# Kernel optimization log

Measured on AMD Instinct MI355X. Metric: run time of the kernel, lower is better.

## Reference

```python
import jax, jax.numpy as jnp
import numpy as np

N = 100000   # nodes
E = 3200000  # edges
D = 128      # in_channels
H = 128      # subhiddens
O = 128      # out_channels
S = 2048     # subgraphs
EPS = 1e-5


def _glorot(k, shape):
    lim = np.sqrt(6.0 / (shape[0] + shape[1])).astype(np.float32)
    return jax.random.uniform(k, shape, jnp.float32, -lim, lim)


def setup_inputs() -> dict:
    key = jax.random.key(0)
    ks = jax.random.split(key, 8)
    x = jax.random.normal(ks[0], (N, D), jnp.float32)
    edge_index = jax.random.randint(ks[1], (2, E), 0, N, dtype=jnp.int32)
    node_to_subgraph = jnp.sort(jax.random.randint(ks[2], (N,), 0, S, dtype=jnp.int32))
    return {
        "x": x,
        "edge_index": edge_index,
        "node_to_subgraph": node_to_subgraph,
        "W1": _glorot(ks[3], (D, H)), "b1": jnp.zeros((H,), jnp.float32),
        "g1": jnp.ones((H,), jnp.float32), "be1": jnp.zeros((H,), jnp.float32),
        "W2": _glorot(ks[4], (H, H)), "b2": jnp.zeros((H,), jnp.float32),
        "g2": jnp.ones((H,), jnp.float32), "be2": jnp.zeros((H,), jnp.float32),
        "W3": _glorot(ks[5], (H, O)), "b3": jnp.zeros((O,), jnp.float32),
    }


def _gcn_conv(x, W, b, row, col, norm):
    # PyG GCNConv: out[col] += norm * (x @ W)[row], then + bias.
    xw = x @ W                                    # [N+?, d] -> [N, d_out]
    msg = xw[row] * norm[:, None]                 # gather over source nodes
    out = jax.ops.segment_sum(msg, col, num_segments=N)
    return out + b


def _bn_relu(x, g, be):
    # BatchNorm1d (training-mode batch stats, biased var) + ReLU
    mean = jnp.mean(x, axis=0)
    var = jnp.mean(jnp.square(x - mean), axis=0)
    return jax.nn.relu((x - mean) * jax.lax.rsqrt(var + EPS) * g + be)


def reference(x, edge_index, node_to_subgraph, W1, b1, g1, be1, W2, b2, g2, be2, W3, b3):
    # GCN symmetric norm with self-loops, shared across the 3 convs.
    loops = jnp.arange(N, dtype=edge_index.dtype)
    row = jnp.concatenate([edge_index[0], loops])  # source
    col = jnp.concatenate([edge_index[1], loops])  # target (aggregation)
    deg = jax.ops.segment_sum(jnp.ones_like(col, dtype=x.dtype), col, num_segments=N)
    dinv = jnp.where(deg > 0, jax.lax.rsqrt(deg), 0.0)
    norm = dinv[row] * dinv[col]

    h1 = _bn_relu(_gcn_conv(x, W1, b1, row, col, norm), g1, be1)   # dropout is no-op in eval
    h2 = _bn_relu(_gcn_conv(h1, W2, b2, row, col, norm), g2, be2)
    h3 = jax.nn.relu(_gcn_conv(h2, W3, b3, row, col, norm))

    cat = jnp.concatenate([h1, h2, h3], axis=-1)                   # [N, 2H+O]
    return jax.ops.segment_max(cat, node_to_subgraph, num_segments=S)  # gmp -> [S, 2H+O]
```

## Files before the change

### kernel.cpp

```cpp
#include <hip/hip_runtime.h>
#include <hip/hip_fp16.h>

#define NN 100000
#define NE 3200000
#define DF 128
#define SG 2048
#define OUTC 384
#define EPS 1e-5f

#define NBUK 800
#define BNODES 125
#define CAP 5120
#define TILE 4096
#define B_BUCKET 782
#define B_GEMM 391
#define LDSTRIDE 136
#define AGG_BLOCKS 2048

typedef _Float16 f16x8 __attribute__((ext_vector_type(8)));
typedef float f32x16 __attribute__((ext_vector_type(16)));

__global__ void k_prepW(const float* __restrict__ W1, const float* __restrict__ W2,
                        const float* __restrict__ W3, __half* __restrict__ WT) {
    const float* W = blockIdx.x == 0 ? W1 : (blockIdx.x == 1 ? W2 : W3);
    __half* out = WT + blockIdx.x * 16384;
    for (int i = threadIdx.x; i < 16384; i += 256) {
        int k = i >> 7, n = i & 127;
        out[n * 128 + k] = __float2half(W[i]);
    }
}

__device__ void bucketA_body(int* smem, int bb,
                             const int* __restrict__ erow, const int* __restrict__ ecol,
                             int* __restrict__ gcur, int* __restrict__ packed) {
    int* sc   = smem;
    int* sr   = smem + 4096;
    int* hist = smem + 8192;
    int* loff = smem + 9216;
    int* gch  = smem + 10240;
    int* cur  = smem + 11264;
    int* psum = smem + 12288;
    int t = threadIdx.x;
    hist[t] = 0; hist[t + 256] = 0; hist[t + 512] = 0; hist[t + 768] = 0;
    __syncthreads();
    int e0 = bb * TILE;
    int lim = NE - e0; if (lim > TILE) lim = TILE;
    for (int i = t; i < lim; i += 256) {
        int c = ecol[e0 + i];
        int r = erow[e0 + i];
        sc[i] = c; sr[i] = r;
        atomicAdd(&hist[c / BNODES], 1);
    }
    __syncthreads();
    int h0 = hist[4 * t], h1 = hist[4 * t + 1], h2 = hist[4 * t + 2], h3 = hist[4 * t + 3];
    int s = h0 + h1 + h2 + h3;
    psum[t] = s; __syncthreads();
    for (int st = 1; st < 256; st <<= 1) {
        int a = (t >= st) ? psum[t - st] : 0;
        __syncthreads();
        psum[t] += a;
        __syncthreads();
    }
    int base = psum[t] - s;
    loff[4 * t] = base;
    loff[4 * t + 1] = base + h0;
    loff[4 * t + 2] = base + h0 + h1;
    loff[4 * t + 3] = base + h0 + h1 + h2;
#pragma unroll
    for (int j = 0; j < 4; ++j) {
        int b = 4 * t + j;
        if (b < NBUK) {
            int c = hist[b];
            gch[b] = c ? atomicAdd(&gcur[b], c) : 0;
            cur[b] = loff[b];
        }
    }
    __syncthreads();
    for (int i = t; i < lim; i += 256) {
        int c = sc[i], r = sr[i];
        int b = c / BNODES;
        int lc = c - b * BNODES;
        int p = atomicAdd(&cur[b], 1);
        int rank = p - loff[b];
        if (gch[b] + rank < CAP) packed[b * CAP + gch[b] + rank] = r | (lc << 17);
    }
}

__device__ void gemm32u_body(int* smem, int gb, const float* __restrict__ A,
                             const __half* __restrict__ WTg, __half* __restrict__ C) {
    _Float16* Wl = (_Float16*)smem;
    int tid = threadIdx.x;
    for (int ch = tid; ch < 2048; ch += 256) {
        int n = ch >> 4, seg = ch & 15;
        *(uint4*)&Wl[n * LDSTRIDE + seg * 8] = *(const uint4*)(WTg + n * 128 + seg * 8);
    }
    __syncthreads();
    int wave = tid >> 6, lane = tid & 63;
    int l31 = lane & 31, lhi = lane >> 5;
    int rowbase = gb * 256 + wave * 64;
    f32x16 acc[2][4];
#pragma unroll
    for (int rt = 0; rt < 2; ++rt)
#pragma unroll
        for (int nt = 0; nt < 4; ++nt)
#pragma unroll
            for (int i = 0; i < 16; ++i) acc[rt][nt][i] = 0.f;
    int r0 = rowbase + l31;      if (r0 >= NN) r0 = NN - 1;
    int r1 = rowbase + 32 + l31; if (r1 >= NN) r1 = NN - 1;
    const float* A0 = A + (size_t)r0 * 128;
    const float* A1 = A + (size_t)r1 * 128;
#pragma unroll
    for (int ks = 0; ks < 8; ++ks) {
        int koff = ks * 16 + lhi * 8;
        float4 f0 = *(const float4*)(A0 + koff);
        float4 f1 = *(const float4*)(A0 + koff + 4);
        float4 g0 = *(const float4*)(A1 + koff);
        float4 g1 = *(const float4*)(A1 + koff + 4);
        f16x8 a0, a1;
        a0[0] = (_Float16)f0.x; a0[1] = (_Float16)f0.y; a0[2] = (_Float16)f0.z; a0[3] = (_Float16)f0.w;
        a0[4] = (_Float16)f1.x; a0[5] = (_Float16)f1.y; a0[6] = (_Float16)f1.z; a0[7] = (_Float16)f1.w;
        a1[0] = (_Float16)g0.x; a1[1] = (_Float16)g0.y; a1[2] = (_Float16)g0.z; a1[3] = (_Float16)g0.w;
        a1[4] = (_Float16)g1.x; a1[5] = (_Float16)g1.y; a1[6] = (_Float16)g1.z; a1[7] = (_Float16)g1.w;
#pragma unroll
        for (int nt = 0; nt < 4; ++nt) {
            f16x8 b = *(const f16x8*)&Wl[(nt * 32 + l31) * LDSTRIDE + ks * 16 + lhi * 8];
            acc[0][nt] = __builtin_amdgcn_mfma_f32_32x32x16_f16(a0, b, acc[0][nt], 0, 0, 0);
            acc[1][nt] = __builtin_amdgcn_mfma_f32_32x32x16_f16(a1, b, acc[1][nt], 0, 0, 0);
        }
    }
#pragma unroll
    for (int rt = 0; rt < 2; ++rt) {
#pragma unroll
        for (int r = 0; r < 16; ++r) {
            int row = rowbase + rt * 32 + (r & 3) + 8 * (r >> 2) + 4 * lhi;
            if (row < NN) {
                size_t cb = (size_t)row * 128 + l31;
                C[cb]      = __float2half(acc[rt][0][r]);
                C[cb + 32] = __float2half(acc[rt][1][r]);
                C[cb + 64] = __float2half(acc[rt][2][r]);
                C[cb + 96] = __float2half(acc[rt][3][r]);
            }
        }
    }
}

__global__ __launch_bounds__(256, 2) void k_fused1(const int* __restrict__ erow,
                                                   const int* __restrict__ ecol,
                                                   int* __restrict__ gcur,
                                                   int* __restrict__ packed,
                                                   const float* __restrict__ x,
                                                   const __half* __restrict__ WT,
                                                   __half* __restrict__ XWh) {
    __shared__ __align__(16) int smem[12544];
    int bb = blockIdx.x;
    if (bb < B_BUCKET) bucketA_body(smem, bb, erow, ecol, gcur, packed);
    else gemm32u_body(smem, bb - B_BUCKET, x, WT, XWh);
}

__global__ __launch_bounds__(256) void k_csrB(int* __restrict__ rows,
                                              const int* __restrict__ gcur,
                                              int* __restrict__ begs, int* __restrict__ ends,
                                              float* __restrict__ dinv) {
    __shared__ int lin[CAP];
    __shared__ int hist[128], off[128], cur[128], psc[128];
    int b = blockIdx.x, t = threadIdx.x;
    int cnt = gcur[b]; if (cnt > CAP) cnt = CAP;
    int base = b * CAP;
    for (int i = t; i < cnt; i += 256) lin[i] = rows[base + i];
    if (t < 128) hist[t] = 0;
    __syncthreads();
    for (int i = t; i < cnt; i += 256) atomicAdd(&hist[lin[i] >> 17], 1);
    __syncthreads();
    int pc = 0;
    if (t < 128) { pc = (hist[t] + 3) & ~3; psc[t] = pc; }
    __syncthreads();
    for (int st = 1; st < 128; st <<= 1) {
        int a = 0;
        if (t < 128 && t >= st) a = psc[t - st];
        __syncthreads();
        if (t < 128) psc[t] += a;
        __syncthreads();
    }
    if (t < 128) { off[t] = psc[t] - pc; cur[t] = off[t]; }
    __syncthreads();
    if (t < BNODES) {
        int n = b * BNODES + t;
        int c = hist[t];
        int bg = base + off[t];
        begs[n] = bg;
        ends[n] = bg + c;
        dinv[n] = rsqrtf((float)(c + 1));
        int pad = (c + 3) & ~3;
        for (int p = c; p < pad; ++p)
            if (off[t] + p < CAP) rows[base + off[t] + p] = 0;
    }
    __syncthreads();
    for (int i = t; i < cnt; i += 256) {
        int w = lin[i];
        int lc = w >> 17;
        int p = atomicAdd(&cur[lc], 1);
        if (p < CAP) rows[base + p] = w & 0x1FFFF;
    }
}

__global__ __launch_bounds__(256, 2) void k_gemm16(const __half* __restrict__ A,
                                                   const __half* __restrict__ WTg,
                                                   const float* __restrict__ dinv,
                                                   __half* __restrict__ C) {
    __shared__ _Float16 Wl[128 * LDSTRIDE];
    int tid = threadIdx.x;
    for (int ch = tid; ch < 2048; ch += 256) {
        int n = ch >> 4, seg = ch & 15;
        *(uint4*)&Wl[n * LDSTRIDE + seg * 8] = *(const uint4*)(WTg + n * 128 + seg * 8);
    }
    __syncthreads();
    int wave = tid >> 6, lane = tid & 63;
    int l31 = lane & 31, lhi = lane >> 5;
    int rowbase = blockIdx.x * 256 + wave * 64;
    f32x16 acc[2][4];
#pragma unroll
    for (int rt = 0; rt < 2; ++rt)
#pragma unroll
        for (int nt = 0; nt < 4; ++nt)
#pragma unroll
            for (int i = 0; i < 16; ++i) acc[rt][nt][i] = 0.f;
    int r0 = rowbase + l31;      if (r0 >= NN) r0 = NN - 1;
    int r1 = rowbase + 32 + l31; if (r1 >= NN) r1 = NN - 1;
    const f16x8* A0 = (const f16x8*)(A + (size_t)r0 * 128);
    const f16x8* A1 = (const f16x8*)(A + (size_t)r1 * 128);
#pragma unroll
    for (int ks = 0; ks < 8; ++ks) {
        f16x8 a0 = A0[ks * 2 + lhi];
        f16x8 a1 = A1[ks * 2 + lhi];
#pragma unroll
        for (int nt = 0; nt < 4; ++nt) {
            f16x8 b = *(const f16x8*)&Wl[(nt * 32 + l31) * LDSTRIDE + ks * 16 + lhi * 8];
            acc[0][nt] = __builtin_amdgcn_mfma_f32_32x32x16_f16(a0, b, acc[0][nt], 0, 0, 0);
            acc[1][nt] = __builtin_amdgcn_mfma_f32_32x32x16_f16(a1, b, acc[1][nt], 0, 0, 0);
        }
    }
#pragma unroll
    for (int rt = 0; rt < 2; ++rt) {
#pragma unroll
        for (int r = 0; r < 16; ++r) {
            int row = rowbase + rt * 32 + (r & 3) + 8 * (r >> 2) + 4 * lhi;
            if (row < NN) {
                float sc = dinv[row];
                size_t cb = (size_t)row * 128 + l31;
                C[cb]      = __float2half(acc[rt][0][r] * sc);
                C[cb + 32] = __float2half(acc[rt][1][r] * sc);
                C[cb + 64] = __float2half(acc[rt][2][r] * sc);
                C[cb + 96] = __float2half(acc[rt][3][r] * sc);
            }
        }
    }
}

__device__ __forceinline__ void accum8(float* acc, uint4 v) {
    float2 f;
    f = __half22float2(*(__half2*)&v.x); acc[0] += f.x; acc[1] += f.y;
    f = __half22float2(*(__half2*)&v.y); acc[2] += f.x; acc[3] += f.y;
    f = __half22float2(*(__half2*)&v.z); acc[4] += f.x; acc[5] += f.y;
    f = __half22float2(*(__half2*)&v.w); acc[6] += f.x; acc[7] += f.y;
}
__device__ __forceinline__ void accum8w(float* acc, uint4 v, float w) {
    float2 f;
    f = __half22float2(*(__half2*)&v.x); acc[0] = fmaf(w, f.x, acc[0]); acc[1] = fmaf(w, f.y, acc[1]);
    f = __half22float2(*(__half2*)&v.y); acc[2] = fmaf(w, f.x, acc[2]); acc[3] = fmaf(w, f.y, acc[3]);
    f = __half22float2(*(__half2*)&v.z); acc[4] = fmaf(w, f.x, acc[4]); acc[5] = fmaf(w, f.y, acc[5]);
    f = __half22float2(*(__half2*)&v.w); acc[6] = fmaf(w, f.x, acc[6]); acc[7] = fmaf(w, f.y, acc[7]);
}

__global__ __launch_bounds__(256) void k_aggh(const __half* __restrict__ XWh,
                                              const int* __restrict__ begs,
                                              const int* __restrict__ ends,
                                              const int* __restrict__ rows,
                                              const float* __restrict__ dinv,
                                              __half* __restrict__ outh) {
    int wid = (blockIdx.x * 256 + threadIdx.x) >> 6;
    int lane = threadIdx.x & 63;
    int quad = lane >> 4, li = lane & 15;
    const uint4* XW4 = (const uint4*)XWh;
    for (int n = wid; n < NN; n += AGG_BLOCKS * 4) {
        float dn = dinv[n];
        int beg = begs[n], end = ends[n];
        float acc[8] = {};
        if (quad == 0) {
            uint4 sv = XW4[(size_t)n * 16 + li];
            accum8(acc, sv);
        }
        int e = beg;
        for (; e + 32 <= end; e += 32) {
            int4 ia = *(const int4*)(rows + e + 4 * quad);
            int4 ib = *(const int4*)(rows + e + 16 + 4 * quad);
            uint4 v0 = XW4[(size_t)ia.x * 16 + li];
            uint4 v1 = XW4[(size_t)ia.y * 16 + li];
            uint4 v2 = XW4[(size_t)ia.z * 16 + li];
            uint4 v3 = XW4[(size_t)ia.w * 16 + li];
            uint4 v4 = XW4[(size_t)ib.x * 16 + li];
            uint4 v5 = XW4[(size_t)ib.y * 16 + li];
            uint4 v6 = XW4[(size_t)ib.z * 16 + li];
            uint4 v7 = XW4[(size_t)ib.w * 16 + li];
            accum8(acc, v0); accum8(acc, v1); accum8(acc, v2); accum8(acc, v3);
            accum8(acc, v4); accum8(acc, v5); accum8(acc, v6); accum8(acc, v7);
        }
        for (; e + 16 <= end; e += 16) {
            int4 ia = *(const int4*)(rows + e + 4 * quad);
            uint4 v0 = XW4[(size_t)ia.x * 16 + li];
            uint4 v1 = XW4[(size_t)ia.y * 16 + li];
            uint4 v2 = XW4[(size_t)ia.z * 16 + li];
            uint4 v3 = XW4[(size_t)ia.w * 16 + li];
            accum8(acc, v0); accum8(acc, v1); accum8(acc, v2); accum8(acc, v3);
        }
        if (e < end) {
            int rem = end - e;
            int qb = 4 * quad;
            int4 it = make_int4(0, 0, 0, 0);
            if (qb < rem) it = *(const int4*)(rows + e + qb);
            uint4 v0 = XW4[(size_t)it.x * 16 + li];
            uint4 v1 = XW4[(size_t)it.y * 16 + li];
            uint4 v2 = XW4[(size_t)it.z * 16 + li];
            uint4 v3 = XW4[(size_t)it.w * 16 + li];
            accum8w(acc, v0, (qb + 0 < rem) ? 1.f : 0.f);
            accum8w(acc, v1, (qb + 1 < rem) ? 1.f : 0.f);
            accum8w(acc, v2, (qb + 2 < rem) ? 1.f : 0.f);
            accum8w(acc, v3, (qb + 3 < rem) ? 1.f : 0.f);
        }
#pragma unroll
        for (int j = 0; j < 8; ++j) {
            acc[j] += __shfl_xor(acc[j], 16, 64);
            acc[j] += __shfl_xor(acc[j], 32, 64);
        }
        if (quad == 0) {
            __half2 h0 = __floats2half2_rn(acc[0] * dn, acc[1] * dn);
            __half2 h1 = __floats2half2_rn(acc[2] * dn, acc[3] * dn);
            __half2 h2 = __floats2half2_rn(acc[4] * dn, acc[5] * dn);
            __half2 h3 = __floats2half2_rn(acc[6] * dn, acc[7] * dn);
            uint4 st;
            st.x = *(unsigned int*)&h0;
            st.y = *(unsigned int*)&h1;
            st.z = *(unsigned int*)&h2;
            st.w = *(unsigned int*)&h3;
            *(uint4*)(outh + (size_t)n * 128 + li * 8) = st;
        }
    }
}

__global__ __launch_bounds__(256) void k_aggh1(const __half* __restrict__ XWh,
                                               const int* __restrict__ begs,
                                               const int* __restrict__ ends,
                                               const int* __restrict__ rows,
                                               const float* __restrict__ dinv,
                                               __half* __restrict__ outh) {
    int wid = (blockIdx.x * 256 + threadIdx.x) >> 6;
    int lane = threadIdx.x & 63;
    int quad = lane >> 4, li = lane & 15;
    const uint4* XW4 = (const uint4*)XWh;
    for (int n = wid; n < NN; n += AGG_BLOCKS * 4) {
        float dn = dinv[n];
        int beg = begs[n], end = ends[n];
        float acc[8] = {};
        if (quad == 0) {
            uint4 sv = XW4[(size_t)n * 16 + li];
            accum8w(acc, sv, dn);
        }
        int e = beg;
        for (; e + 16 <= end; e += 16) {
            int4 ia = *(const int4*)(rows + e + 4 * quad);
            float d0 = dinv[ia.x];
            float d1 = dinv[ia.y];
            float d2 = dinv[ia.z];
            float d3 = dinv[ia.w];
            uint4 v0 = XW4[(size_t)ia.x * 16 + li];
            uint4 v1 = XW4[(size_t)ia.y * 16 + li];
            uint4 v2 = XW4[(size_t)ia.z * 16 + li];
            uint4 v3 = XW4[(size_t)ia.w * 16 + li];
            accum8w(acc, v0, d0); accum8w(acc, v1, d1);
            accum8w(acc, v2, d2); accum8w(acc, v3, d3);
        }
        if (e < end) {
            int rem = end - e;
            int qb = 4 * quad;
            int4 it = make_int4(0, 0, 0, 0);
            if (qb < rem) it = *(const int4*)(rows + e + qb);
            float d0 = (qb + 0 < rem) ? dinv[it.x] : 0.f;
            float d1 = (qb + 1 < rem) ? dinv[it.y] : 0.f;
            float d2 = (qb + 2 < rem) ? dinv[it.z] : 0.f;
            float d3 = (qb + 3 < rem) ? dinv[it.w] : 0.f;
            uint4 v0 = XW4[(size_t)it.x * 16 + li];
            uint4 v1 = XW4[(size_t)it.y * 16 + li];
            uint4 v2 = XW4[(size_t)it.z * 16 + li];
            uint4 v3 = XW4[(size_t)it.w * 16 + li];
            accum8w(acc, v0, d0); accum8w(acc, v1, d1);
            accum8w(acc, v2, d2); accum8w(acc, v3, d3);
        }
#pragma unroll
        for (int j = 0; j < 8; ++j) {
            acc[j] += __shfl_xor(acc[j], 16, 64);
            acc[j] += __shfl_xor(acc[j], 32, 64);
        }
        if (quad == 0) {
            __half2 h0 = __floats2half2_rn(acc[0] * dn, acc[1] * dn);
            __half2 h1 = __floats2half2_rn(acc[2] * dn, acc[3] * dn);
            __half2 h2 = __floats2half2_rn(acc[4] * dn, acc[5] * dn);
            __half2 h3 = __floats2half2_rn(acc[6] * dn, acc[7] * dn);
            uint4 st;
            st.x = *(unsigned int*)&h0;
            st.y = *(unsigned int*)&h1;
            st.z = *(unsigned int*)&h2;
            st.w = *(unsigned int*)&h3;
            *(uint4*)(outh + (size_t)n * 128 + li * 8) = st;
        }
    }
}

__global__ void k_stats(const __half* __restrict__ buf, float* __restrict__ sums) {
    int c = threadIdx.x & 127;
    int rg = threadIdx.x >> 7;
    float s = 0.f, q = 0.f;
    for (int r = blockIdx.x * 2 + rg; r < NN; r += gridDim.x * 2) {
        float v = __half2float(buf[(size_t)r * 128 + c]);
        s += v; q += v * v;
    }
    __shared__ float sh[512];
    sh[threadIdx.x] = s;
    sh[256 + threadIdx.x] = q;
    __syncthreads();
    if (threadIdx.x < 128) {
        s = sh[threadIdx.x] + sh[threadIdx.x + 128];
        q = sh[256 + threadIdx.x] + sh[256 + threadIdx.x + 128];
        atomicAdd(&sums[threadIdx.x], s);
        atomicAdd(&sums[128 + threadIdx.x], q);
    }
}

__global__ void k_bnmax(__half* __restrict__ buf, const float* __restrict__ sums,
                        const float* __restrict__ g, const float* __restrict__ be,
                        const int* __restrict__ n2s,
                        unsigned int* __restrict__ outmax, int colOff) {
    int c = threadIdx.x & 127;
    int rg = threadIdx.x >> 7;
    int n0 = blockIdx.x * 64;
    int nEnd = n0 + 64; if (nEnd > NN) nEnd = NN;
    float mean = sums[c] * (1.0f / NN);
    float inv = rsqrtf(sums[128 + c] * (1.0f / NN) - mean * mean + EPS) * g[c];
    float sc = inv, sh = be[c] - mean * inv;
    int cur = -1; float runmax = 0.f;
    for (int n = n0 + rg; n < nEnd; n += 2) {
        float v = fmaxf(__half2float(buf[(size_t)n * 128 + c]) * sc + sh, 0.f);
        buf[(size_t)n * 128 + c] = __float2half(v);
        int sg = n2s[n];
        if (sg != cur) {
            if (cur >= 0) atomicMax(&outmax[cur * OUTC + colOff + c], __float_as_uint(runmax));
            cur = sg; runmax = v;
        } else {
            runmax = fmaxf(runmax, v);
        }
    }
    if (cur >= 0) atomicMax(&outmax[cur * OUTC + colOff + c], __float_as_uint(runmax));
}

__global__ void k_biasmax(const __half* __restrict__ buf, const float* __restrict__ b3,
                          const int* __restrict__ n2s,
                          unsigned int* __restrict__ outmax, int colOff) {
    int c = threadIdx.x & 127;
    int rg = threadIdx.x >> 7;
    int n0 = blockIdx.x * 64;
    int nEnd = n0 + 64; if (nEnd > NN) nEnd = NN;
    float bias = b3[c];
    int cur = -1; float runmax = 0.f;
    for (int n = n0 + rg; n < nEnd; n += 2) {
        float v = fmaxf(__half2float(buf[(size_t)n * 128 + c]) + bias, 0.f);
        int sg = n2s[n];
        if (sg != cur) {
            if (cur >= 0) atomicMax(&outmax[cur * OUTC + colOff + c], __float_as_uint(runmax));
            cur = sg; runmax = v;
        } else {
            runmax = fmaxf(runmax, v);
        }
    }
    if (cur >= 0) atomicMax(&outmax[cur * OUTC + colOff + c], __float_as_uint(runmax));
}

extern "C" void kernel_launch(void* const* d_in, const int* in_sizes, int n_in,
                              void* d_out, int out_size, void* d_ws, size_t ws_size,
                              hipStream_t stream) {
    const float* x   = (const float*)d_in[0];
    const int*   ei  = (const int*)d_in[1];
    const int*   n2s = (const int*)d_in[2];
    const float* W1  = (const float*)d_in[3];
    const float* g1  = (const float*)d_in[5];
    const float* be1 = (const float*)d_in[6];
    const float* W2  = (const float*)d_in[7];
    const float* g2  = (const float*)d_in[9];
    const float* be2 = (const float*)d_in[10];
    const float* W3  = (const float*)d_in[11];
    const float* b3  = (const float*)d_in[12];

    __half* H    = (__half*)d_ws;
    __half* XWh  = H + (size_t)NN * 128;
    __half* WT   = XWh + (size_t)NN * 128;
    int* rows    = (int*)(WT + 3 * 16384);
    int* begs    = rows + (size_t)NBUK * CAP;
    int* ends    = begs + NN;
    float* dinv  = (float*)(ends + NN);
    int* gcur    = (int*)(dinv + NN);
    float* sums  = (float*)(gcur + NBUK);

    const int* erow = ei;
    const int* ecol = ei + NE;

    hipMemsetAsync(gcur, 0, (NBUK + 512) * sizeof(int), stream);
    hipMemsetAsync(d_out, 0, (size_t)out_size * sizeof(float), stream);

    k_prepW<<<3, 256, 0, stream>>>(W1, W2, W3, WT);
    k_fused1<<<B_BUCKET + B_GEMM, 256, 0, stream>>>(erow, ecol, gcur, rows, x, WT, XWh);
    k_csrB<<<NBUK, 256, 0, stream>>>(rows, gcur, begs, ends, dinv);

    unsigned int* outmax = (unsigned int*)d_out;
    int nbSeg = (NN + 63) / 64;
    int nbG = (NN + 255) / 256;

    k_aggh1<<<AGG_BLOCKS, 256, 0, stream>>>(XWh, begs, ends, rows, dinv, H);
    k_stats<<<512, 256, 0, stream>>>(H, sums);
    k_bnmax<<<nbSeg, 256, 0, stream>>>(H, sums, g1, be1, n2s, outmax, 0);

    k_gemm16<<<nbG, 256, 0, stream>>>(H, WT + 16384, dinv, XWh);
    k_aggh<<<AGG_BLOCKS, 256, 0, stream>>>(XWh, begs, ends, rows, dinv, H);
    k_stats<<<512, 256, 0, stream>>>(H, sums + 256);
    k_bnmax<<<nbSeg, 256, 0, stream>>>(H, sums + 256, g2, be2, n2s, outmax, 128);

    k_gemm16<<<nbG, 256, 0, stream>>>(H, WT + 32768, dinv, XWh);
    k_aggh<<<AGG_BLOCKS, 256, 0, stream>>>(XWh, begs, ends, rows, dinv, H);
    k_biasmax<<<nbSeg, 256, 0, stream>>>(H, b3, n2s, outmax, 256);
}
```

Baseline: 745.3 us.

## Fuse BN stats and final max-pool into aggregation; pre-scale XW by dinv

BatchNorm sum and sum-of-squares statistics are now accumulated inside the aggregation kernel. The separate stats pass over the hidden buffer goes away. The third aggregation applies bias, ReLU and the subgraph segment-max directly, so the final activation is never written out. The first-layer XW rows are pre-scaled by dinv in the CSR build kernel, which removes the per-edge dinv gathers. Memsets and weight prep are merged into one init kernel, and nodes are assigned to waves in contiguous chunks of 13, which gives less even load balancing.

```diff
diff --git a/kernel.cpp b/kernel.cpp
--- a/kernel.cpp
+++ b/kernel.cpp
@@ -16,17 +16,26 @@
 #define B_GEMM 391
 #define LDSTRIDE 136
 #define AGG_BLOCKS 2048
+#define AGG_WAVES (AGG_BLOCKS * 4)
+#define CHUNK 13
 
 typedef _Float16 f16x8 __attribute__((ext_vector_type(8)));
 typedef float f32x16 __attribute__((ext_vector_type(16)));
 
-__global__ void k_prepW(const float* __restrict__ W1, const float* __restrict__ W2,
-                        const float* __restrict__ W3, __half* __restrict__ WT) {
-    const float* W = blockIdx.x == 0 ? W1 : (blockIdx.x == 1 ? W2 : W3);
-    __half* out = WT + blockIdx.x * 16384;
-    for (int i = threadIdx.x; i < 16384; i += 256) {
-        int k = i >> 7, n = i & 127;
-        out[n * 128 + k] = __float2half(W[i]);
+__global__ void k_init(const float* __restrict__ W1, const float* __restrict__ W2,
+                       const float* __restrict__ W3, __half* __restrict__ WT,
+                       unsigned int* __restrict__ outz, int* __restrict__ gcur,
+                       float* __restrict__ sums) {
+    int g = blockIdx.x * 256 + threadIdx.x;
+    int nt = gridDim.x * 256;
+    for (int i = g; i < SG * OUTC; i += nt) outz[i] = 0u;
+    if (g < NBUK) gcur[g] = 0;
+    if (g < 512) sums[g] = 0.f;
+    for (int i = g; i < 3 * 16384; i += nt) {
+        int m = i >> 14, idx = i & 16383;
+        int k = idx >> 7, n = idx & 127;
+        const float* W = m == 0 ? W1 : (m == 1 ? W2 : W3);
+        WT[m * 16384 + n * 128 + k] = __float2half(W[idx]);
     }
 }
 
@@ -160,9 +169,11 @@
 __global__ __launch_bounds__(256) void k_csrB(int* __restrict__ rows,
                                               const int* __restrict__ gcur,
                                               int* __restrict__ begs, int* __restrict__ ends,
-                                              float* __restrict__ dinv) {
+                                              float* __restrict__ dinv,
+                                              __half* __restrict__ XWh) {
     __shared__ int lin[CAP];
     __shared__ int hist[128], off[128], cur[128], psc[128];
+    __shared__ float dinvl[128];
     int b = blockIdx.x, t = threadIdx.x;
     int cnt = gcur[b]; if (cnt > CAP) cnt = CAP;
     int base = b * CAP;
@@ -189,7 +200,9 @@
         int bg = base + off[t];
         begs[n] = bg;
         ends[n] = bg + c;
-        dinv[n] = rsqrtf((float)(c + 1));
+        float dv = rsqrtf((float)(c + 1));
+        dinv[n] = dv;
+        dinvl[t] = dv;
         int pad = (c + 3) & ~3;
         for (int p = c; p < pad; ++p)
             if (off[t] + p < CAP) rows[base + off[t] + p] = 0;
@@ -200,6 +213,23 @@
         int lc = w >> 17;
         int p = atomicAdd(&cur[lc], 1);
         if (p < CAP) rows[base + p] = w & 0x1FFFF;
+    }
+    int rr = t >> 1, half = t & 1;
+    if (rr < BNODES) {
+        float dv = dinvl[rr];
+        int n = b * BNODES + rr;
+        uint4* p = (uint4*)(XWh + (size_t)n * 128) + half * 8;
+#pragma unroll
+        for (int j = 0; j < 8; ++j) {
+            uint4 v = p[j];
+            __half2* h = (__half2*)&v;
+#pragma unroll
+            for (int q = 0; q < 4; ++q) {
+                float2 f = __half22float2(h[q]);
+                h[q] = __floats2half2_rn(f.x * dv, f.y * dv);
+            }
+            p[j] = v;
+        }
     }
 }
 
@@ -271,166 +301,150 @@
     f = __half22float2(*(__half2*)&v.w); acc[6] = fmaf(w, f.x, acc[6]); acc[7] = fmaf(w, f.y, acc[7]);
 }
 
-__global__ __launch_bounds__(256) void k_aggh(const __half* __restrict__ XWh,
-                                              const int* __restrict__ begs,
-                                              const int* __restrict__ ends,
-                                              const int* __restrict__ rows,
-                                              const float* __restrict__ dinv,
-                                              __half* __restrict__ outh) {
-    int wid = (blockIdx.x * 256 + threadIdx.x) >> 6;
-    int lane = threadIdx.x & 63;
-    int quad = lane >> 4, li = lane & 15;
-    const uint4* XW4 = (const uint4*)XWh;
-    for (int n = wid; n < NN; n += AGG_BLOCKS * 4) {
-        float dn = dinv[n];
-        int beg = begs[n], end = ends[n];
-        float acc[8] = {};
-        if (quad == 0) {
-            uint4 sv = XW4[(size_t)n * 16 + li];
-            accum8(acc, sv);
-        }
-        int e = beg;
-        for (; e + 32 <= end; e += 32) {
-            int4 ia = *(const int4*)(rows + e + 4 * quad);
-            int4 ib = *(const int4*)(rows + e + 16 + 4 * quad);
-            uint4 v0 = XW4[(size_t)ia.x * 16 + li];
-            uint4 v1 = XW4[(size_t)ia.y * 16 + li];
-            uint4 v2 = XW4[(size_t)ia.z * 16 + li];
-            uint4 v3 = XW4[(size_t)ia.w * 16 + li];
-            uint4 v4 = XW4[(size_t)ib.x * 16 + li];
-            uint4 v5 = XW4[(size_t)ib.y * 16 + li];
-            uint4 v6 = XW4[(size_t)ib.z * 16 + li];
-            uint4 v7 = XW4[(size_t)ib.w * 16 + li];
-            accum8(acc, v0); accum8(acc, v1); accum8(acc, v2); accum8(acc, v3);
-            accum8(acc, v4); accum8(acc, v5); accum8(acc, v6); accum8(acc, v7);
-        }
-        for (; e + 16 <= end; e += 16) {
-            int4 ia = *(const int4*)(rows + e + 4 * quad);
-            uint4 v0 = XW4[(size_t)ia.x * 16 + li];
-            uint4 v1 = XW4[(size_t)ia.y * 16 + li];
-            uint4 v2 = XW4[(size_t)ia.z * 16 + li];
-            uint4 v3 = XW4[(size_t)ia.w * 16 + li];
-            accum8(acc, v0); accum8(acc, v1); accum8(acc, v2); accum8(acc, v3);
-        }
-        if (e < end) {
-            int rem = end - e;
-            int qb = 4 * quad;
-            int4 it = make_int4(0, 0, 0, 0);
-            if (qb < rem) it = *(const int4*)(rows + e + qb);
-            uint4 v0 = XW4[(size_t)it.x * 16 + li];
-            uint4 v1 = XW4[(size_t)it.y * 16 + li];
-            uint4 v2 = XW4[(size_t)it.z * 16 + li];
-            uint4 v3 = XW4[(size_t)it.w * 16 + li];
-            accum8w(acc, v0, (qb + 0 < rem) ? 1.f : 0.f);
-            accum8w(acc, v1, (qb + 1 < rem) ? 1.f : 0.f);
-            accum8w(acc, v2, (qb + 2 < rem) ? 1.f : 0.f);
-            accum8w(acc, v3, (qb + 3 < rem) ? 1.f : 0.f);
-        }
-#pragma unroll
-        for (int j = 0; j < 8; ++j) {
-            acc[j] += __shfl_xor(acc[j], 16, 64);
-            acc[j] += __shfl_xor(acc[j], 32, 64);
-        }
-        if (quad == 0) {
-            __half2 h0 = __floats2half2_rn(acc[0] * dn, acc[1] * dn);
-            __half2 h1 = __floats2half2_rn(acc[2] * dn, acc[3] * dn);
-            __half2 h2 = __floats2half2_rn(acc[4] * dn, acc[5] * dn);
-            __half2 h3 = __floats2half2_rn(acc[6] * dn, acc[7] * dn);
-            uint4 st;
-            st.x = *(unsigned int*)&h0;
-            st.y = *(unsigned int*)&h1;
-            st.z = *(unsigned int*)&h2;
-            st.w = *(unsigned int*)&h3;
-            *(uint4*)(outh + (size_t)n * 128 + li * 8) = st;
-        }
-    }
-}
-
-__global__ __launch_bounds__(256) void k_aggh1(const __half* __restrict__ XWh,
+__device__ __forceinline__ void agg_node(const uint4* __restrict__ XW4,
+                                         const int* __restrict__ rows,
+                                         int n, int beg, int end, int quad, int li,
+                                         float* acc) {
+#pragma unroll
+    for (int j = 0; j < 8; ++j) acc[j] = 0.f;
+    if (quad == 0) {
+        uint4 sv = XW4[(size_t)n * 16 + li];
+        accum8(acc, sv);
+    }
+    int e = beg;
+    for (; e + 32 <= end; e += 32) {
+        int4 ia = *(const int4*)(rows + e + 4 * quad);
+        int4 ib = *(const int4*)(rows + e + 16 + 4 * quad);
+        uint4 v0 = XW4[(size_t)ia.x * 16 + li];
+        uint4 v1 = XW4[(size_t)ia.y * 16 + li];
+        uint4 v2 = XW4[(size_t)ia.z * 16 + li];
+        uint4 v3 = XW4[(size_t)ia.w * 16 + li];
+        uint4 v4 = XW4[(size_t)ib.x * 16 + li];
+        uint4 v5 = XW4[(size_t)ib.y * 16 + li];
+        uint4 v6 = XW4[(size_t)ib.z * 16 + li];
+        uint4 v7 = XW4[(size_t)ib.w * 16 + li];
+        accum8(acc, v0); accum8(acc, v1); accum8(acc, v2); accum8(acc, v3);
+        accum8(acc, v4); accum8(acc, v5); accum8(acc, v6); accum8(acc, v7);
+    }
+    for (; e + 16 <= end; e += 16) {
+        int4 ia = *(const int4*)(rows + e + 4 * quad);
+        uint4 v0 = XW4[(size_t)ia.x * 16 + li];
+        uint4 v1 = XW4[(size_t)ia.y * 16 + li];
+        uint4 v2 = XW4[(size_t)ia.z * 16 + li];
+        uint4 v3 = XW4[(size_t)ia.w * 16 + li];
+        accum8(acc, v0); accum8(acc, v1); accum8(acc, v2); accum8(acc, v3);
+    }
+    if (e < end) {
+        int rem = end - e;
+        int qb = 4 * quad;
+        int4 it = make_int4(0, 0, 0, 0);
+        if (qb < rem) it = *(const int4*)(rows + e + qb);
+        uint4 v0 = XW4[(size_t)it.x * 16 + li];
+        uint4 v1 = XW4[(size_t)it.y * 16 + li];
+        uint4 v2 = XW4[(size_t)it.z * 16 + li];
+        uint4 v3 = XW4[(size_t)it.w * 16 + li];
+        accum8w(acc, v0, (qb + 0 < rem) ? 1.f : 0.f);
+        accum8w(acc, v1, (qb + 1 < rem) ? 1.f : 0.f);
+        accum8w(acc, v2, (qb + 2 < rem) ? 1.f : 0.f);
+        accum8w(acc, v3, (qb + 3 < rem) ? 1.f : 0.f);
+    }
+#pragma unroll
+    for (int j = 0; j < 8; ++j) {
+        acc[j] += __shfl_xor(acc[j], 16, 64);
+        acc[j] += __shfl_xor(acc[j], 32, 64);
+    }
+}
+
+__global__ __launch_bounds__(256) void k_agghs(const __half* __restrict__ XWh,
                                                const int* __restrict__ begs,
                                                const int* __restrict__ ends,
                                                const int* __restrict__ rows,
                                                const float* __restrict__ dinv,
-                                               __half* __restrict__ outh) {
-    int wid = (blockIdx.x * 256 + threadIdx.x) >> 6;
-    int lane = threadIdx.x & 63;
+                                               __half* __restrict__ outh,
+                                               float* __restrict__ sums) {
+    __shared__ float sred[4][256];
+    int wave = threadIdx.x >> 6, lane = threadIdx.x & 63;
     int quad = lane >> 4, li = lane & 15;
     const uint4* XW4 = (const uint4*)XWh;
-    for (int n = wid; n < NN; n += AGG_BLOCKS * 4) {
+    int wid = blockIdx.x * 4 + wave;
+    int n0 = wid * CHUNK;
+    int n1 = n0 + CHUNK; if (n1 > NN) n1 = NN;
+    float ssum[8] = {}, sqsum[8] = {};
+    for (int n = n0; n < n1; ++n) {
+        float acc[8];
+        agg_node(XW4, rows, n, begs[n], ends[n], quad, li, acc);
+        if (quad == 0) {
+            float dn = dinv[n];
+            __half2 hh[4];
+#pragma unroll
+            for (int j = 0; j < 8; ++j) {
+                float v = acc[j] * dn;
+                acc[j] = v;
+                ssum[j] += v;
+                sqsum[j] += v * v;
+            }
+            hh[0] = __floats2half2_rn(acc[0], acc[1]);
+            hh[1] = __floats2half2_rn(acc[2], acc[3]);
+            hh[2] = __floats2half2_rn(acc[4], acc[5]);
+            hh[3] = __floats2half2_rn(acc[6], acc[7]);
+            *(uint4*)(outh + (size_t)n * 128 + li * 8) = *(uint4*)hh;
+        }
+    }
+    if (quad == 0) {
+#pragma unroll
+        for (int j = 0; j < 8; ++j) {
+            sred[wave][li * 8 + j] = ssum[j];
+            sred[wave][128 + li * 8 + j] = sqsum[j];
+        }
+    }
+    __syncthreads();
+    int t = threadIdx.x;
+    float tot = sred[0][t] + sred[1][t] + sred[2][t] + sred[3][t];
+    atomicAdd(&sums[t], tot);
+}
+
+__global__ __launch_bounds__(256) void k_agghmax(const __half* __restrict__ XWh,
+                                                 const int* __restrict__ begs,
+                                                 const int* __restrict__ ends,
+                                                 const int* __restrict__ rows,
+                                                 const float* __restrict__ dinv,
+                                                 const float* __restrict__ b3,
+                                                 const int* __restrict__ n2s,
+                                                 unsigned int* __restrict__ outmax) {
+    int wave = threadIdx.x >> 6, lane = threadIdx.x & 63;
+    int quad = lane >> 4, li = lane & 15;
+    const uint4* XW4 = (const uint4*)XWh;
+    int wid = blockIdx.x * 4 + wave;
+    int n0 = wid * CHUNK;
+    int n1 = n0 + CHUNK; if (n1 > NN) n1 = NN;
+    float4 bz0 = *(const float4*)(b3 + li * 8);
+    float4 bz1 = *(const float4*)(b3 + li * 8 + 4);
+    float bias[8] = {bz0.x, bz0.y, bz0.z, bz0.w, bz1.x, bz1.y, bz1.z, bz1.w};
+    int cur = -1;
+    float runmax[8];
+    for (int n = n0; n < n1; ++n) {
+        float acc[8];
+        agg_node(XW4, rows, n, begs[n], ends[n], quad, li, acc);
         float dn = dinv[n];
-        int beg = begs[n], end = ends[n];
-        float acc[8] = {};
-        if (quad == 0) {
-            uint4 sv = XW4[(size_t)n * 16 + li];
-            accum8w(acc, sv, dn);
-        }
-        int e = beg;
-        for (; e + 16 <= end; e += 16) {
-            int4 ia = *(const int4*)(rows + e + 4 * quad);
-            float d0 = dinv[ia.x];
-            float d1 = dinv[ia.y];
-            float d2 = dinv[ia.z];
-            float d3 = dinv[ia.w];
-            uint4 v0 = XW4[(size_t)ia.x * 16 + li];
-            uint4 v1 = XW4[(size_t)ia.y * 16 + li];
-            uint4 v2 = XW4[(size_t)ia.z * 16 + li];
-            uint4 v3 = XW4[(size_t)ia.w * 16 + li];
-            accum8w(acc, v0, d0); accum8w(acc, v1, d1);
-            accum8w(acc, v2, d2); accum8w(acc, v3, d3);
-        }
-        if (e < end) {
-            int rem = end - e;
-            int qb = 4 * quad;
-            int4 it = make_int4(0, 0, 0, 0);
-            if (qb < rem) it = *(const int4*)(rows + e + qb);
-            float d0 = (qb + 0 < rem) ? dinv[it.x] : 0.f;
-            float d1 = (qb + 1 < rem) ? dinv[it.y] : 0.f;
-            float d2 = (qb + 2 < rem) ? dinv[it.z] : 0.f;
-            float d3 = (qb + 3 < rem) ? dinv[it.w] : 0.f;
-            uint4 v0 = XW4[(size_t)it.x * 16 + li];
-            uint4 v1 = XW4[(size_t)it.y * 16 + li];
-            uint4 v2 = XW4[(size_t)it.z * 16 + li];
-            uint4 v3 = XW4[(size_t)it.w * 16 + li];
-            accum8w(acc, v0, d0); accum8w(acc, v1, d1);
-            accum8w(acc, v2, d2); accum8w(acc, v3, d3);
-        }
-#pragma unroll
-        for (int j = 0; j < 8; ++j) {
-            acc[j] += __shfl_xor(acc[j], 16, 64);
-            acc[j] += __shfl_xor(acc[j], 32, 64);
-        }
-        if (quad == 0) {
-            __half2 h0 = __floats2half2_rn(acc[0] * dn, acc[1] * dn);
-            __half2 h1 = __floats2half2_rn(acc[2] * dn, acc[3] * dn);
-            __half2 h2 = __floats2half2_rn(acc[4] * dn, acc[5] * dn);
-            __half2 h3 = __floats2half2_rn(acc[6] * dn, acc[7] * dn);
-            uint4 st;
-            st.x = *(unsigned int*)&h0;
-            st.y = *(unsigned int*)&h1;
-            st.z = *(unsigned int*)&h2;
-            st.w = *(unsigned int*)&h3;
-            *(uint4*)(outh + (size_t)n * 128 + li * 8) = st;
-        }
-    }
-}
-
-__global__ void k_stats(const __half* __restrict__ buf, float* __restrict__ sums) {
-    int c = threadIdx.x & 127;
-    int rg = threadIdx.x >> 7;
-    float s = 0.f, q = 0.f;
-    for (int r = blockIdx.x * 2 + rg; r < NN; r += gridDim.x * 2) {
-        float v = __half2float(buf[(size_t)r * 128 + c]);
-        s += v; q += v * v;
-    }
-    __shared__ float sh[512];
-    sh[threadIdx.x] = s;
-    sh[256 + threadIdx.x] = q;
-    __syncthreads();
-    if (threadIdx.x < 128) {
-        s = sh[threadIdx.x] + sh[threadIdx.x + 128];
-        q = sh[256 + threadIdx.x] + sh[256 + threadIdx.x + 128];
-        atomicAdd(&sums[threadIdx.x], s);
-        atomicAdd(&sums[128 + threadIdx.x], q);
+        int sg = n2s[n];
+        if (sg != cur) {
+            if (cur >= 0 && quad == 0) {
+#pragma unroll
+                for (int j = 0; j < 8; ++j)
+                    atomicMax(&outmax[cur * OUTC + 256 + li * 8 + j], __float_as_uint(runmax[j]));
+            }
+            cur = sg;
+#pragma unroll
+            for (int j = 0; j < 8; ++j) runmax[j] = fmaxf(acc[j] * dn + bias[j], 0.f);
+        } else {
+#pragma unroll
+            for (int j = 0; j < 8; ++j) runmax[j] = fmaxf(runmax[j], fmaxf(acc[j] * dn + bias[j], 0.f));
+        }
+    }
+    if (cur >= 0 && quad == 0) {
+#pragma unroll
+        for (int j = 0; j < 8; ++j)
+            atomicMax(&outmax[cur * OUTC + 256 + li * 8 + j], __float_as_uint(runmax[j]));
     }
 }
 
@@ -460,28 +474,6 @@
     if (cur >= 0) atomicMax(&outmax[cur * OUTC + colOff + c], __float_as_uint(runmax));
 }
 
-__global__ void k_biasmax(const __half* __restrict__ buf, const float* __restrict__ b3,
-                          const int* __restrict__ n2s,
-                          unsigned int* __restrict__ outmax, int colOff) {
-    int c = threadIdx.x & 127;
-    int rg = threadIdx.x >> 7;
-    int n0 = blockIdx.x * 64;
-    int nEnd = n0 + 64; if (nEnd > NN) nEnd = NN;
-    float bias = b3[c];
-    int cur = -1; float runmax = 0.f;
-    for (int n = n0 + rg; n < nEnd; n += 2) {
-        float v = fmaxf(__half2float(buf[(size_t)n * 128 + c]) + bias, 0.f);
-        int sg = n2s[n];
-        if (sg != cur) {
-            if (cur >= 0) atomicMax(&outmax[cur * OUTC + colOff + c], __float_as_uint(runmax));
-            cur = sg; runmax = v;
-        } else {
-            runmax = fmaxf(runmax, v);
-        }
-    }
-    if (cur >= 0) atomicMax(&outmax[cur * OUTC + colOff + c], __float_as_uint(runmax));
-}
-
 extern "C" void kernel_launch(void* const* d_in, const int* in_sizes, int n_in,
                               void* d_out, int out_size, void* d_ws, size_t ws_size,
                               hipStream_t stream) {
@@ -509,28 +501,21 @@
 
     const int* erow = ei;
     const int* ecol = ei + NE;
-
-    hipMemsetAsync(gcur, 0, (NBUK + 512) * sizeof(int), stream);
-    hipMemsetAsync(d_out, 0, (size_t)out_size * sizeof(float), stream);
-
-    k_prepW<<<3, 256, 0, stream>>>(W1, W2, W3, WT);
-    k_fused1<<<B_BUCKET + B_GEMM, 256, 0, stream>>>(erow, ecol, gcur, rows, x, WT, XWh);
-    k_csrB<<<NBUK, 256, 0, stream>>>(rows, gcur, begs, ends, dinv);
-
     unsigned int* outmax = (unsigned int*)d_out;
     int nbSeg = (NN + 63) / 64;
     int nbG = (NN + 255) / 256;
 
-    k_aggh1<<<AGG_BLOCKS, 256, 0, stream>>>(XWh, begs, ends, rows, dinv, H);
-    k_stats<<<512, 256, 0, stream>>>(H, sums);
+    k_init<<<512, 256, 0, stream>>>(W1, W2, W3, WT, outmax, gcur, sums);
+    k_fused1<<<B_BUCKET + B_GEMM, 256, 0, stream>>>(erow, ecol, gcur, rows, x, WT, XWh);
+    k_csrB<<<NBUK, 256, 0, stream>>>(rows, gcur, begs, ends, dinv, XWh);
+
+    k_agghs<<<AGG_BLOCKS, 256, 0, stream>>>(XWh, begs, ends, rows, dinv, H, sums);
     k_bnmax<<<nbSeg, 256, 0, stream>>>(H, sums, g1, be1, n2s, outmax, 0);
 
     k_gemm16<<<nbG, 256, 0, stream>>>(H, WT + 16384, dinv, XWh);
-    k_aggh<<<AGG_BLOCKS, 256, 0, stream>>>(XWh, begs, ends, rows, dinv, H);
-    k_stats<<<512, 256, 0, stream>>>(H, sums + 256);
+    k_agghs<<<AGG_BLOCKS, 256, 0, stream>>>(XWh, begs, ends, rows, dinv, H, sums + 256);
     k_bnmax<<<nbSeg, 256, 0, stream>>>(H, sums + 256, g2, be2, n2s, outmax, 128);
 
     k_gemm16<<<nbG, 256, 0, stream>>>(H, WT + 32768, dinv, XWh);
-    k_aggh<<<AGG_BLOCKS, 256, 0, stream>>>(XWh, begs, ends, rows, dinv, H);
-    k_biasmax<<<nbSeg, 256, 0, stream>>>(H, b3, n2s, outmax, 256);
-}
+    k_agghmax<<<AGG_BLOCKS, 256, 0, stream>>>(XWh, begs, ends, rows, dinv, b3, n2s, outmax);
+}
```

Result: faster. 705.4 us (-5.4%).
